# Kernel optimization log

Hardware: AMD Instinct MI355X
Metric: run time of the kernel (lower is better)

The kernel has to match this reference:

```python
import jax, jax.numpy as jnp
import numpy as np

B, N, D, W = 4, 4096, 256, 7
K = 2 * W + 1  # 15 taps: positions [i-2w, ..., i]
H = 4 * D
EPS = 1e-5


def layer_norm(x, g, b):
    mu = jnp.mean(x, axis=-1, keepdims=True)
    var = jnp.mean(jnp.square(x - mu), axis=-1, keepdims=True)
    return (x - mu) * jax.lax.rsqrt(var + EPS) * g + b


def setup_inputs() -> dict:
    key = jax.random.key(0)
    ks = jax.random.split(key, 8)
    s = 0.02
    return {
        "x": jax.random.normal(ks[0], (B, N, D), dtype=jnp.float32),
        # w_mix[k] is the DxD block of the (K*D -> D) Linear acting on offset k-2w
        "w_mix": (jax.random.normal(ks[1], (K, D, D), dtype=jnp.float32) * s),
        "b_mix": jnp.zeros((D,), dtype=jnp.float32),
        "g1": jnp.ones((D,), jnp.float32) + 0.1 * jax.random.normal(ks[2], (D,), jnp.float32),
        "b1": 0.1 * jax.random.normal(ks[3], (D,), jnp.float32),
        "w_ff1": jax.random.normal(ks[4], (D, H), dtype=jnp.float32) * s,
        "b_ff1": jnp.zeros((H,), dtype=jnp.float32),
        "w_ff2": jax.random.normal(ks[5], (H, D), dtype=jnp.float32) * s,
        "b_ff2": jnp.zeros((D,), dtype=jnp.float32),
        "g2": jnp.ones((D,), jnp.float32) + 0.1 * jax.random.normal(ks[6], (D,), jnp.float32),
        "b2": 0.1 * jax.random.normal(ks[7], (D,), jnp.float32),
    }


def reference(x, w_mix, b_mix, g1, b1, w_ff1, b_ff1, w_ff2, b_ff2, g2, b2):
    # Causal windowed concat + Linear == causal 1D conv with kernel K=2w+1.
    # torch feats chunk k holds x[i - 2w + k]; conv tap k with left pad 2w
    # sees exactly x[i - 2w + k], so kernel = mix weight reshaped (K, D, D).
    mix = jax.lax.conv_general_dilated(
        x, w_mix, window_strides=(1,), padding=[(2 * W, 0)],
        dimension_numbers=("NWC", "WIO", "NWC"),
    ) + b_mix  # [B, N, D]
    # Dropout is identity in eval mode (reference baseline).
    h = layer_norm(x + mix, g1, b1)
    ff = jnp.dot(jax.nn.gelu(jnp.dot(h, w_ff1) + b_ff1, approximate=False), w_ff2) + b_ff2
    return layer_norm(h + ff, g2, b2)
```

## Files before the change

kernel.cpp:

```cpp
#include <hip/hip_runtime.h>
#include <cstdint>

#define DD     256
#define HH     1024
#define NNSEQ  4096
#define KDIM   3840
#define NSTEPS 120
#define MT     64
#define XROWS  78
#define XPITCH 264
#define APITCH 136
#define EPSLN  1e-5f

typedef unsigned short u16;
typedef __attribute__((ext_vector_type(8))) short short8;
typedef __attribute__((ext_vector_type(4))) float f32x4;

#define MFMA(a, b, c) __builtin_amdgcn_mfma_f32_16x16x32_bf16(a, b, c, 0, 0, 0)

__device__ __forceinline__ u16 f2bf(float f) {
  unsigned u = __float_as_uint(f);
  u += 0x7FFF + ((u >> 16) & 1);
  return (u16)(u >> 16);
}
__device__ __forceinline__ float bf2f(u16 s) { return __uint_as_float(((unsigned)s) << 16); }

__global__ __launch_bounds__(256) void k_prep(
    const float* __restrict__ wmix, const float* __restrict__ wff1,
    const float* __restrict__ wff2, u16* __restrict__ wpk,
    u16* __restrict__ w1pk, u16* __restrict__ w2pk)
{
  __shared__ float t[32][257];
  const int b = blockIdx.x, tid = threadIdx.x;

  if (b < 120) {
    const int s = b;
    for (int r = 0; r < 32; ++r)
      t[r][tid] = wmix[(size_t)(s * 32 + r) * 256 + tid];
    __syncthreads();
#pragma unroll
    for (int f = 0; f < 4; ++f) {
      const int l = tid & 63, q = l >> 4, cl = l & 15;
      const int nt = (tid >> 6) & 3, ng = f;
      const int n = ng * 64 + nt * 16 + cl;
      uint4 pk;
      unsigned* p = (unsigned*)&pk;
#pragma unroll
      for (int jj = 0; jj < 4; ++jj)
        p[jj] = (unsigned)f2bf(t[q * 8 + jj * 2][n]) | ((unsigned)f2bf(t[q * 8 + jj * 2 + 1][n]) << 16);
      *(uint4*)&wpk[((size_t)s * 1024 + f * 256 + tid) * 8] = pk;
    }
  } else if (b < 184) {
    const int u = b - 120, c = u >> 3, s = u & 7;
    for (int i = 0; i < 16; ++i) {
      const int r = i * 2 + (tid >> 7), col = tid & 127;
      t[r][col] = wff1[(size_t)(s * 32 + r) * 1024 + c * 128 + col];
    }
    __syncthreads();
#pragma unroll
    for (int f = 0; f < 2; ++f) {
      const int l = tid & 63, q = l >> 4, cl = l & 15;
      const int nt = (tid >> 6) & 1, ng = f * 2 + (tid >> 7);
      const int n = ng * 32 + nt * 16 + cl;
      uint4 pk;
      unsigned* p = (unsigned*)&pk;
#pragma unroll
      for (int jj = 0; jj < 4; ++jj)
        p[jj] = (unsigned)f2bf(t[q * 8 + jj * 2][n]) | ((unsigned)f2bf(t[q * 8 + jj * 2 + 1][n]) << 16);
      *(uint4*)&w1pk[((size_t)(c * 8 + s) * 512 + f * 256 + tid) * 8] = pk;
    }
  } else {
    const int u = b - 184, c = u >> 2, s = u & 3;
    for (int r = 0; r < 32; ++r)
      t[r][tid] = wff2[(size_t)(c * 128 + s * 32 + r) * 256 + tid];
    __syncthreads();
#pragma unroll
    for (int f = 0; f < 4; ++f) {
      const int l = tid & 63, q = l >> 4, cl = l & 15;
      const int nt = (tid >> 6) & 3, ng = f;
      const int n = ng * 64 + nt * 16 + cl;
      uint4 pk;
      unsigned* p = (unsigned*)&pk;
#pragma unroll
      for (int jj = 0; jj < 4; ++jj)
        p[jj] = (unsigned)f2bf(t[q * 8 + jj * 2][n]) | ((unsigned)f2bf(t[q * 8 + jj * 2 + 1][n]) << 16);
      *(uint4*)&w2pk[((size_t)(c * 4 + s) * 1024 + f * 256 + tid) * 8] = pk;
    }
  }
}

__global__ __launch_bounds__(512) void k_mix_ln1(
    const float* __restrict__ x, const u16* __restrict__ wpk,
    const float* __restrict__ bmix, const float* __restrict__ g1,
    const float* __restrict__ b1, u16* __restrict__ h)
{
  __shared__ u16 xs[XROWS * XPITCH];
  __shared__ float redS[4][64], redS2[4][64];
  __shared__ float muL[64], invL[64];

  const int tid = threadIdx.x;
  const int wv = tid >> 6, l = tid & 63, q = l >> 4, cl = l & 15;
  const int mg = wv >> 2, ng = wv & 3;
  const long tok0 = (long)blockIdx.x * MT;
  const int n0 = (int)(tok0 & (NNSEQ - 1));

  {
    const int cslot = (tid & 63) * 4;
    for (int r = tid >> 6; r < XROWS; r += 8) {
      const int nloc = n0 - 14 + r;
      float4 v = make_float4(0.f, 0.f, 0.f, 0.f);
      if (nloc >= 0) v = *(const float4*)&x[(tok0 - 14 + r) * DD + cslot];
      uint2 pk;
      pk.x = (unsigned)f2bf(v.x) | ((unsigned)f2bf(v.y) << 16);
      pk.y = (unsigned)f2bf(v.z) | ((unsigned)f2bf(v.w) << 16);
      *(uint2*)&xs[r * XPITCH + cslot] = pk;
    }
  }
  __syncthreads();

  f32x4 acc[2][4];
#pragma unroll
  for (int nt = 0; nt < 4; ++nt) {
    const float bm = bmix[ng * 64 + nt * 16 + cl];
#pragma unroll
    for (int mt = 0; mt < 2; ++mt) acc[mt][nt] = (f32x4){bm, bm, bm, bm};
  }

  const u16* bbase = wpk + (size_t)(ng * 4) * 512 + (size_t)l * 8;

#define LOAD_A(dst, s_)                                                        \
  {                                                                            \
    const int xrow = (s_) >> 3, c0 = ((s_) & 7) * 32;                          \
    _Pragma("unroll")                                                          \
    for (int mt = 0; mt < 2; ++mt)                                             \
      dst[mt] = *(const short8*)&xs[(xrow + mg * 32 + mt * 16 + cl) * XPITCH + c0 + q * 8]; \
  }
#define LOAD_B(dst, s_)                                                        \
  {                                                                            \
    const u16* bp = bbase + (size_t)(s_) * 8192;                               \
    _Pragma("unroll")                                                          \
    for (int nt = 0; nt < 4; ++nt)                                             \
      dst[nt] = *(const short8*)(bp + nt * 512);                               \
  }

  short8 af[3][2], bfr[3][4];
  LOAD_A(af[0], 0) LOAD_B(bfr[0], 0)
  LOAD_A(af[1], 1) LOAD_B(bfr[1], 1)
  LOAD_A(af[2], 2) LOAD_B(bfr[2], 2)

#pragma unroll 3
  for (int s = 0; s < NSTEPS; ++s) {
    const int cur = s % 3;
#pragma unroll
    for (int mt = 0; mt < 2; ++mt)
#pragma unroll
      for (int nt = 0; nt < 4; ++nt)
        acc[mt][nt] = MFMA(af[cur][mt], bfr[cur][nt], acc[mt][nt]);
    if (s + 3 < NSTEPS) {
      LOAD_A(af[cur], s + 3)
      LOAD_B(bfr[cur], s + 3)
    }
  }

#pragma unroll
  for (int mt = 0; mt < 2; ++mt)
#pragma unroll
    for (int nt = 0; nt < 4; ++nt) {
      const int col = ng * 64 + nt * 16 + cl;
#pragma unroll
      for (int reg = 0; reg < 4; ++reg) {
        const int row = mg * 32 + mt * 16 + q * 4 + reg;
        acc[mt][nt][reg] += x[(tok0 + row) * DD + col];
      }
    }

  float ps[2][4], ps2[2][4];
#pragma unroll
  for (int mt = 0; mt < 2; ++mt)
#pragma unroll
    for (int reg = 0; reg < 4; ++reg) {
      float s = 0.f, s2 = 0.f;
#pragma unroll
      for (int nt = 0; nt < 4; ++nt) { const float y = acc[mt][nt][reg]; s += y; s2 += y * y; }
#pragma unroll
      for (int off = 1; off < 16; off <<= 1) { s += __shfl_xor(s, off, 64); s2 += __shfl_xor(s2, off, 64); }
      ps[mt][reg] = s; ps2[mt][reg] = s2;
    }
  if (cl == 0) {
#pragma unroll
    for (int mt = 0; mt < 2; ++mt)
#pragma unroll
      for (int reg = 0; reg < 4; ++reg) {
        const int row = mg * 32 + mt * 16 + q * 4 + reg;
        redS[ng][row] = ps[mt][reg]; redS2[ng][row] = ps2[mt][reg];
      }
  }
  __syncthreads();
  if (tid < 64) {
    const float s  = redS[0][tid] + redS[1][tid] + redS[2][tid] + redS[3][tid];
    const float s2 = redS2[0][tid] + redS2[1][tid] + redS2[2][tid] + redS2[3][tid];
    const float mu = s * (1.f / DD);
    const float var = s2 * (1.f / DD) - mu * mu;
    muL[tid] = mu; invL[tid] = rsqrtf(var + EPSLN);
  }
  __syncthreads();

#pragma unroll
  for (int nt = 0; nt < 4; ++nt) {
    const int col = ng * 64 + nt * 16 + cl;
    const float gv = g1[col], bv = b1[col];
#pragma unroll
    for (int mt = 0; mt < 2; ++mt)
#pragma unroll
      for (int reg = 0; reg < 4; ++reg) {
        const int row = mg * 32 + mt * 16 + q * 4 + reg;
        const float hv = (acc[mt][nt][reg] - muL[row]) * invL[row] * gv + bv;
        h[(tok0 + row) * DD + col] = f2bf(hv);
      }
  }
#undef LOAD_A
#undef LOAD_B
}

__global__ __launch_bounds__(512) void k_ffn_ln2(
    const u16* __restrict__ h, const u16* __restrict__ w1pk,
    const float* __restrict__ bf1, const u16* __restrict__ w2pk,
    const float* __restrict__ bf2, const float* __restrict__ g2,
    const float* __restrict__ b2, float* __restrict__ out)
{
  __shared__ u16 hs[64 * XPITCH];
  __shared__ u16 asb[64 * APITCH];
  __shared__ float redS[4][64], redS2[4][64];
  __shared__ float muL[64], invL[64];

  const int tid = threadIdx.x;
  const int wv = tid >> 6, l = tid & 63, q = l >> 4, cl = l & 15;
  const int mg = wv >> 2, ng = wv & 3;
  const long tok0 = (long)blockIdx.x * MT;

  {
    const int chunk = tid & 31;
#pragma unroll
    for (int i = 0; i < 4; ++i) {
      const int row = (tid >> 5) + i * 16;
      const uint4 v = *(const uint4*)&h[(tok0 + row) * DD + chunk * 8];
      *(uint4*)&hs[row * XPITCH + chunk * 8] = v;
    }
  }
  __syncthreads();

  f32x4 acc2[2][4];
#pragma unroll
  for (int nt = 0; nt < 4; ++nt) {
    const float bv = bf2[ng * 64 + nt * 16 + cl];
#pragma unroll
    for (int mt = 0; mt < 2; ++mt) acc2[mt][nt] = (f32x4){bv, bv, bv, bv};
  }

  for (int c = 0; c < 8; ++c) {
    f32x4 acc1[2][2];
#pragma unroll
    for (int nt = 0; nt < 2; ++nt) {
      const float bv = bf1[c * 128 + ng * 32 + nt * 16 + cl];
#pragma unroll
      for (int mt = 0; mt < 2; ++mt) acc1[mt][nt] = (f32x4){bv, bv, bv, bv};
    }
#pragma unroll
    for (int s = 0; s < 8; ++s) {
      short8 a[2], b[2];
#pragma unroll
      for (int mt = 0; mt < 2; ++mt)
        a[mt] = *(const short8*)&hs[(mg * 32 + mt * 16 + cl) * XPITCH + s * 32 + q * 8];
      const u16* bp = w1pk + ((size_t)((c * 8 + s) * 4 + ng) * 2) * 512 + (size_t)l * 8;
#pragma unroll
      for (int nt = 0; nt < 2; ++nt)
        b[nt] = *(const short8*)(bp + nt * 512);
#pragma unroll
      for (int mt = 0; mt < 2; ++mt)
#pragma unroll
        for (int nt = 0; nt < 2; ++nt)
          acc1[mt][nt] = MFMA(a[mt], b[nt], acc1[mt][nt]);
    }
#pragma unroll
    for (int mt = 0; mt < 2; ++mt)
#pragma unroll
      for (int nt = 0; nt < 2; ++nt)
#pragma unroll
        for (int reg = 0; reg < 4; ++reg) {
          const float v = acc1[mt][nt][reg];
          const float g = 0.5f * v * (1.f + erff(v * 0.70710678118654752f));
          asb[(mg * 32 + mt * 16 + q * 4 + reg) * APITCH + ng * 32 + nt * 16 + cl] = f2bf(g);
        }
    __syncthreads();
#pragma unroll
    for (int s = 0; s < 4; ++s) {
      short8 a[2], b[4];
#pragma unroll
      for (int mt = 0; mt < 2; ++mt)
        a[mt] = *(const short8*)&asb[(mg * 32 + mt * 16 + cl) * APITCH + s * 32 + q * 8];
      const u16* bp = w2pk + ((size_t)((c * 4 + s) * 4 + ng) * 4) * 512 + (size_t)l * 8;
#pragma unroll
      for (int nt = 0; nt < 4; ++nt)
        b[nt] = *(const short8*)(bp + nt * 512);
#pragma unroll
      for (int mt = 0; mt < 2; ++mt)
#pragma unroll
        for (int nt = 0; nt < 4; ++nt)
          acc2[mt][nt] = MFMA(a[mt], b[nt], acc2[mt][nt]);
    }
    __syncthreads();
  }

#pragma unroll
  for (int mt = 0; mt < 2; ++mt)
#pragma unroll
    for (int nt = 0; nt < 4; ++nt) {
      const int col = ng * 64 + nt * 16 + cl;
#pragma unroll
      for (int reg = 0; reg < 4; ++reg) {
        const int row = mg * 32 + mt * 16 + q * 4 + reg;
        acc2[mt][nt][reg] += bf2f(hs[row * XPITCH + col]);
      }
    }

  float ps[2][4], ps2[2][4];
#pragma unroll
  for (int mt = 0; mt < 2; ++mt)
#pragma unroll
    for (int reg = 0; reg < 4; ++reg) {
      float s = 0.f, s2 = 0.f;
#pragma unroll
      for (int nt = 0; nt < 4; ++nt) { const float y = acc2[mt][nt][reg]; s += y; s2 += y * y; }
#pragma unroll
      for (int off = 1; off < 16; off <<= 1) { s += __shfl_xor(s, off, 64); s2 += __shfl_xor(s2, off, 64); }
      ps[mt][reg] = s; ps2[mt][reg] = s2;
    }
  if (cl == 0) {
#pragma unroll
    for (int mt = 0; mt < 2; ++mt)
#pragma unroll
      for (int reg = 0; reg < 4; ++reg) {
        const int row = mg * 32 + mt * 16 + q * 4 + reg;
        redS[ng][row] = ps[mt][reg]; redS2[ng][row] = ps2[mt][reg];
      }
  }
  __syncthreads();
  if (tid < 64) {
    const float s  = redS[0][tid] + redS[1][tid] + redS[2][tid] + redS[3][tid];
    const float s2 = redS2[0][tid] + redS2[1][tid] + redS2[2][tid] + redS2[3][tid];
    const float mu = s * (1.f / DD);
    const float var = s2 * (1.f / DD) - mu * mu;
    muL[tid] = mu; invL[tid] = rsqrtf(var + EPSLN);
  }
  __syncthreads();

#pragma unroll
  for (int nt = 0; nt < 4; ++nt) {
    const int col = ng * 64 + nt * 16 + cl;
    const float gv = g2[col], bv = b2[col];
#pragma unroll
    for (int mt = 0; mt < 2; ++mt)
#pragma unroll
      for (int reg = 0; reg < 4; ++reg) {
        const int row = mg * 32 + mt * 16 + q * 4 + reg;
        out[(tok0 + row) * DD + col] = (acc2[mt][nt][reg] - muL[row]) * invL[row] * gv + bv;
      }
  }
}

extern "C" void kernel_launch(void* const* d_in, const int* in_sizes, int n_in,
                              void* d_out, int out_size, void* d_ws, size_t ws_size,
                              hipStream_t stream) {
  const float* x    = (const float*)d_in[0];
  const float* wmix = (const float*)d_in[1];
  const float* bmix = (const float*)d_in[2];
  const float* g1   = (const float*)d_in[3];
  const float* b1   = (const float*)d_in[4];
  const float* wff1 = (const float*)d_in[5];
  const float* bff1 = (const float*)d_in[6];
  const float* wff2 = (const float*)d_in[7];
  const float* bff2 = (const float*)d_in[8];
  const float* g2   = (const float*)d_in[9];
  const float* b2   = (const float*)d_in[10];
  float* out = (float*)d_out;

  u16* wpk  = (u16*)d_ws;
  u16* w1pk = wpk + 983040;
  u16* w2pk = w1pk + 262144;
  u16* hb   = w2pk + 262144;

  k_prep<<<216, 256, 0, stream>>>(wmix, wff1, wff2, wpk, w1pk, w2pk);

  const int R = 4 * NNSEQ;
  k_mix_ln1 <<<R / MT, 512, 0, stream>>>(x, wpk, bmix, g1, b1, hb);
  k_ffn_ln2 <<<R / MT, 512, 0, stream>>>(hb, w1pk, bff1, w2pk, bff2, g2, b2, out);
}
```

Measured before the change: 174.0 us.

## Use four waves per block, each covering all 64 rows to reuse B fragments

Both fused kernels drop from 512 to 256 threads. Each of the 4 waves now owns a 64-column slice across all 64 rows, instead of 8 waves splitting rows into two groups. This halves the global weight-fragment loads per block, since each B fragment now feeds 4 row tiles instead of 2. The cost is doubled accumulator and A-fragment registers per wave and fewer waves per block to hide latency.

Measured after the change: 186.9 us. 1.07x slower.

```diff
diff --git a/kernel.cpp b/kernel.cpp
--- a/kernel.cpp
+++ b/kernel.cpp
@@ -89,7 +89,7 @@
   }
 }
 
-__global__ __launch_bounds__(512) void k_mix_ln1(
+__global__ __launch_bounds__(256) void k_mix_ln1(
     const float* __restrict__ x, const u16* __restrict__ wpk,
     const float* __restrict__ bmix, const float* __restrict__ g1,
     const float* __restrict__ b1, u16* __restrict__ h)
@@ -99,14 +99,13 @@
   __shared__ float muL[64], invL[64];
 
   const int tid = threadIdx.x;
-  const int wv = tid >> 6, l = tid & 63, q = l >> 4, cl = l & 15;
-  const int mg = wv >> 2, ng = wv & 3;
+  const int ng = tid >> 6, l = tid & 63, q = l >> 4, cl = l & 15;
   const long tok0 = (long)blockIdx.x * MT;
   const int n0 = (int)(tok0 & (NNSEQ - 1));
 
   {
     const int cslot = (tid & 63) * 4;
-    for (int r = tid >> 6; r < XROWS; r += 8) {
+    for (int r = tid >> 6; r < XROWS; r += 4) {
       const int nloc = n0 - 14 + r;
       float4 v = make_float4(0.f, 0.f, 0.f, 0.f);
       if (nloc >= 0) v = *(const float4*)&x[(tok0 - 14 + r) * DD + cslot];
@@ -118,22 +117,22 @@
   }
   __syncthreads();
 
-  f32x4 acc[2][4];
+  f32x4 acc[4][4];
 #pragma unroll
   for (int nt = 0; nt < 4; ++nt) {
     const float bm = bmix[ng * 64 + nt * 16 + cl];
 #pragma unroll
-    for (int mt = 0; mt < 2; ++mt) acc[mt][nt] = (f32x4){bm, bm, bm, bm};
-  }
-
-  const u16* bbase = wpk + (size_t)(ng * 4) * 512 + (size_t)l * 8;
+    for (int mt = 0; mt < 4; ++mt) acc[mt][nt] = (f32x4){bm, bm, bm, bm};
+  }
+
+  const u16* bbase = wpk + (size_t)ng * 2048 + (size_t)l * 8;
 
 #define LOAD_A(dst, s_)                                                        \
   {                                                                            \
     const int xrow = (s_) >> 3, c0 = ((s_) & 7) * 32;                          \
     _Pragma("unroll")                                                          \
-    for (int mt = 0; mt < 2; ++mt)                                             \
-      dst[mt] = *(const short8*)&xs[(xrow + mg * 32 + mt * 16 + cl) * XPITCH + c0 + q * 8]; \
+    for (int mt = 0; mt < 4; ++mt)                                             \
+      dst[mt] = *(const short8*)&xs[(xrow + mt * 16 + cl) * XPITCH + c0 + q * 8]; \
   }
 #define LOAD_B(dst, s_)                                                        \
   {                                                                            \
@@ -143,7 +142,7 @@
       dst[nt] = *(const short8*)(bp + nt * 512);                               \
   }
 
-  short8 af[3][2], bfr[3][4];
+  short8 af[3][4], bfr[3][4];
   LOAD_A(af[0], 0) LOAD_B(bfr[0], 0)
   LOAD_A(af[1], 1) LOAD_B(bfr[1], 1)
   LOAD_A(af[2], 2) LOAD_B(bfr[2], 2)
@@ -152,7 +151,7 @@
   for (int s = 0; s < NSTEPS; ++s) {
     const int cur = s % 3;
 #pragma unroll
-    for (int mt = 0; mt < 2; ++mt)
+    for (int mt = 0; mt < 4; ++mt)
 #pragma unroll
       for (int nt = 0; nt < 4; ++nt)
         acc[mt][nt] = MFMA(af[cur][mt], bfr[cur][nt], acc[mt][nt]);
@@ -161,22 +160,24 @@
       LOAD_B(bfr[cur], s + 3)
     }
   }
-
-#pragma unroll
-  for (int mt = 0; mt < 2; ++mt)
+#undef LOAD_A
+#undef LOAD_B
+
+#pragma unroll
+  for (int mt = 0; mt < 4; ++mt)
 #pragma unroll
     for (int nt = 0; nt < 4; ++nt) {
       const int col = ng * 64 + nt * 16 + cl;
 #pragma unroll
       for (int reg = 0; reg < 4; ++reg) {
-        const int row = mg * 32 + mt * 16 + q * 4 + reg;
+        const int row = mt * 16 + q * 4 + reg;
         acc[mt][nt][reg] += x[(tok0 + row) * DD + col];
       }
     }
 
-  float ps[2][4], ps2[2][4];
-#pragma unroll
-  for (int mt = 0; mt < 2; ++mt)
+  float ps[4][4], ps2[4][4];
+#pragma unroll
+  for (int mt = 0; mt < 4; ++mt)
 #pragma unroll
     for (int reg = 0; reg < 4; ++reg) {
       float s = 0.f, s2 = 0.f;
@@ -188,10 +189,10 @@
     }
   if (cl == 0) {
 #pragma unroll
-    for (int mt = 0; mt < 2; ++mt)
-#pragma unroll
-      for (int reg = 0; reg < 4; ++reg) {
-        const int row = mg * 32 + mt * 16 + q * 4 + reg;
+    for (int mt = 0; mt < 4; ++mt)
+#pragma unroll
+      for (int reg = 0; reg < 4; ++reg) {
+        const int row = mt * 16 + q * 4 + reg;
         redS[ng][row] = ps[mt][reg]; redS2[ng][row] = ps2[mt][reg];
       }
   }
@@ -210,19 +211,17 @@
     const int col = ng * 64 + nt * 16 + cl;
     const float gv = g1[col], bv = b1[col];
 #pragma unroll
-    for (int mt = 0; mt < 2; ++mt)
-#pragma unroll
-      for (int reg = 0; reg < 4; ++reg) {
-        const int row = mg * 32 + mt * 16 + q * 4 + reg;
+    for (int mt = 0; mt < 4; ++mt)
+#pragma unroll
+      for (int reg = 0; reg < 4; ++reg) {
+        const int row = mt * 16 + q * 4 + reg;
         const float hv = (acc[mt][nt][reg] - muL[row]) * invL[row] * gv + bv;
         h[(tok0 + row) * DD + col] = f2bf(hv);
       }
   }
-#undef LOAD_A
-#undef LOAD_B
-}
-
-__global__ __launch_bounds__(512) void k_ffn_ln2(
+}
+
+__global__ __launch_bounds__(256) void k_ffn_ln2(
     const u16* __restrict__ h, const u16* __restrict__ w1pk,
     const float* __restrict__ bf1, const u16* __restrict__ w2pk,
     const float* __restrict__ bf2, const float* __restrict__ g2,
@@ -234,76 +233,75 @@
   __shared__ float muL[64], invL[64];
 
   const int tid = threadIdx.x;
-  const int wv = tid >> 6, l = tid & 63, q = l >> 4, cl = l & 15;
-  const int mg = wv >> 2, ng = wv & 3;
+  const int ng = tid >> 6, l = tid & 63, q = l >> 4, cl = l & 15;
   const long tok0 = (long)blockIdx.x * MT;
 
   {
     const int chunk = tid & 31;
 #pragma unroll
-    for (int i = 0; i < 4; ++i) {
-      const int row = (tid >> 5) + i * 16;
+    for (int i = 0; i < 8; ++i) {
+      const int row = (tid >> 5) + i * 8;
       const uint4 v = *(const uint4*)&h[(tok0 + row) * DD + chunk * 8];
       *(uint4*)&hs[row * XPITCH + chunk * 8] = v;
     }
   }
   __syncthreads();
 
-  f32x4 acc2[2][4];
+  f32x4 acc2[4][4];
 #pragma unroll
   for (int nt = 0; nt < 4; ++nt) {
     const float bv = bf2[ng * 64 + nt * 16 + cl];
 #pragma unroll
-    for (int mt = 0; mt < 2; ++mt) acc2[mt][nt] = (f32x4){bv, bv, bv, bv};
+    for (int mt = 0; mt < 4; ++mt) acc2[mt][nt] = (f32x4){bv, bv, bv, bv};
   }
 
   for (int c = 0; c < 8; ++c) {
-    f32x4 acc1[2][2];
+    f32x4 acc1[4][2];
 #pragma unroll
     for (int nt = 0; nt < 2; ++nt) {
       const float bv = bf1[c * 128 + ng * 32 + nt * 16 + cl];
 #pragma unroll
-      for (int mt = 0; mt < 2; ++mt) acc1[mt][nt] = (f32x4){bv, bv, bv, bv};
+      for (int mt = 0; mt < 4; ++mt) acc1[mt][nt] = (f32x4){bv, bv, bv, bv};
     }
 #pragma unroll
     for (int s = 0; s < 8; ++s) {
-      short8 a[2], b[2];
-#pragma unroll
-      for (int mt = 0; mt < 2; ++mt)
-        a[mt] = *(const short8*)&hs[(mg * 32 + mt * 16 + cl) * XPITCH + s * 32 + q * 8];
-      const u16* bp = w1pk + ((size_t)((c * 8 + s) * 4 + ng) * 2) * 512 + (size_t)l * 8;
+      short8 a[4], b[2];
+#pragma unroll
+      for (int mt = 0; mt < 4; ++mt)
+        a[mt] = *(const short8*)&hs[(mt * 16 + cl) * XPITCH + s * 32 + q * 8];
+      const u16* bp = w1pk + (size_t)(c * 8 + s) * 4096 + ng * 1024 + (size_t)l * 8;
 #pragma unroll
       for (int nt = 0; nt < 2; ++nt)
         b[nt] = *(const short8*)(bp + nt * 512);
 #pragma unroll
-      for (int mt = 0; mt < 2; ++mt)
+      for (int mt = 0; mt < 4; ++mt)
 #pragma unroll
         for (int nt = 0; nt < 2; ++nt)
           acc1[mt][nt] = MFMA(a[mt], b[nt], acc1[mt][nt]);
     }
 #pragma unroll
-    for (int mt = 0; mt < 2; ++mt)
+    for (int mt = 0; mt < 4; ++mt)
 #pragma unroll
       for (int nt = 0; nt < 2; ++nt)
 #pragma unroll
         for (int reg = 0; reg < 4; ++reg) {
           const float v = acc1[mt][nt][reg];
           const float g = 0.5f * v * (1.f + erff(v * 0.70710678118654752f));
-          asb[(mg * 32 + mt * 16 + q * 4 + reg) * APITCH + ng * 32 + nt * 16 + cl] = f2bf(g);
+          asb[(mt * 16 + q * 4 + reg) * APITCH + ng * 32 + nt * 16 + cl] = f2bf(g);
         }
     __syncthreads();
 #pragma unroll
     for (int s = 0; s < 4; ++s) {
-      short8 a[2], b[4];
-#pragma unroll
-      for (int mt = 0; mt < 2; ++mt)
-        a[mt] = *(const short8*)&asb[(mg * 32 + mt * 16 + cl) * APITCH + s * 32 + q * 8];
-      const u16* bp = w2pk + ((size_t)((c * 4 + s) * 4 + ng) * 4) * 512 + (size_t)l * 8;
+      short8 a[4], b[4];
+#pragma unroll
+      for (int mt = 0; mt < 4; ++mt)
+        a[mt] = *(const short8*)&asb[(mt * 16 + cl) * APITCH + s * 32 + q * 8];
+      const u16* bp = w2pk + (size_t)(c * 4 + s) * 8192 + ng * 2048 + (size_t)l * 8;
 #pragma unroll
       for (int nt = 0; nt < 4; ++nt)
         b[nt] = *(const short8*)(bp + nt * 512);
 #pragma unroll
-      for (int mt = 0; mt < 2; ++mt)
+      for (int mt = 0; mt < 4; ++mt)
 #pragma unroll
         for (int nt = 0; nt < 4; ++nt)
           acc2[mt][nt] = MFMA(a[mt], b[nt], acc2[mt][nt]);
@@ -312,20 +310,20 @@
   }
 
 #pragma unroll
-  for (int mt = 0; mt < 2; ++mt)
+  for (int mt = 0; mt < 4; ++mt)
 #pragma unroll
     for (int nt = 0; nt < 4; ++nt) {
       const int col = ng * 64 + nt * 16 + cl;
 #pragma unroll
       for (int reg = 0; reg < 4; ++reg) {
-        const int row = mg * 32 + mt * 16 + q * 4 + reg;
+        const int row = mt * 16 + q * 4 + reg;
         acc2[mt][nt][reg] += bf2f(hs[row * XPITCH + col]);
       }
     }
 
-  float ps[2][4], ps2[2][4];
-#pragma unroll
-  for (int mt = 0; mt < 2; ++mt)
+  float ps[4][4], ps2[4][4];
+#pragma unroll
+  for (int mt = 0; mt < 4; ++mt)
 #pragma unroll
     for (int reg = 0; reg < 4; ++reg) {
       float s = 0.f, s2 = 0.f;
@@ -337,10 +335,10 @@
     }
   if (cl == 0) {
 #pragma unroll
-    for (int mt = 0; mt < 2; ++mt)
-#pragma unroll
-      for (int reg = 0; reg < 4; ++reg) {
-        const int row = mg * 32 + mt * 16 + q * 4 + reg;
+    for (int mt = 0; mt < 4; ++mt)
+#pragma unroll
+      for (int reg = 0; reg < 4; ++reg) {
+        const int row = mt * 16 + q * 4 + reg;
         redS[ng][row] = ps[mt][reg]; redS2[ng][row] = ps2[mt][reg];
       }
   }
@@ -359,10 +357,10 @@
     const int col = ng * 64 + nt * 16 + cl;
     const float gv = g2[col], bv = b2[col];
 #pragma unroll
-    for (int mt = 0; mt < 2; ++mt)
-#pragma unroll
-      for (int reg = 0; reg < 4; ++reg) {
-        const int row = mg * 32 + mt * 16 + q * 4 + reg;
+    for (int mt = 0; mt < 4; ++mt)
+#pragma unroll
+      for (int reg = 0; reg < 4; ++reg) {
+        const int row = mt * 16 + q * 4 + reg;
         out[(tok0 + row) * DD + col] = (acc2[mt][nt][reg] - muL[row]) * invL[row] * gv + bv;
       }
   }
@@ -392,6 +390,6 @@
   k_prep<<<216, 256, 0, stream>>>(wmix, wff1, wff2, wpk, w1pk, w2pk);
 
   const int R = 4 * NNSEQ;
-  k_mix_ln1 <<<R / MT, 512, 0, stream>>>(x, wpk, bmix, g1, b1, hb);
-  k_ffn_ln2 <<<R / MT, 512, 0, stream>>>(hb, w1pk, bff1, w2pk, bff2, g2, b2, out);
-}
+  k_mix_ln1 <<<R / MT, 256, 0, stream>>>(x, wpk, bmix, g1, b1, hb);
+  k_ffn_ln2 <<<R / MT, 256, 0, stream>>>(hb, w1pk, bff1, w2pk, bff2, g2, b2, out);
+}
```

## Fuse mix+LN1 and FFN+LN2 into one kernel with unified weight packing

Applied to the files above, without the earlier changes.

Merges the two main kernels so the LN1 output h stays in shared memory as bf16 and feeds the FFN directly. This removes the global write and read of h and one kernel launch. The FFN hidden dimension is now processed in chunks of 256 instead of 128, and all three weight packings share one 256-column layout and one code path in the prep kernel. Launch bounds now request 2 blocks per CU, which caps register use. Shared memory per block grows, which may limit occupancy and cause spills.

After: 168.1 us. 1.03x faster.

```diff
diff --git a/kernel.cpp b/kernel.cpp
--- a/kernel.cpp
+++ b/kernel.cpp
@@ -9,7 +9,6 @@
 #define MT     64
 #define XROWS  78
 #define XPITCH 264
-#define APITCH 136
 #define EPSLN  1e-5f
 
 typedef unsigned short u16;
@@ -33,68 +32,48 @@
   __shared__ float t[32][257];
   const int b = blockIdx.x, tid = threadIdx.x;
 
+  u16* dst;
   if (b < 120) {
-    const int s = b;
+    dst = wpk + (size_t)b * 8192;
     for (int r = 0; r < 32; ++r)
-      t[r][tid] = wmix[(size_t)(s * 32 + r) * 256 + tid];
-    __syncthreads();
-#pragma unroll
-    for (int f = 0; f < 4; ++f) {
-      const int l = tid & 63, q = l >> 4, cl = l & 15;
-      const int nt = (tid >> 6) & 3, ng = f;
-      const int n = ng * 64 + nt * 16 + cl;
-      uint4 pk;
-      unsigned* p = (unsigned*)&pk;
-#pragma unroll
-      for (int jj = 0; jj < 4; ++jj)
-        p[jj] = (unsigned)f2bf(t[q * 8 + jj * 2][n]) | ((unsigned)f2bf(t[q * 8 + jj * 2 + 1][n]) << 16);
-      *(uint4*)&wpk[((size_t)s * 1024 + f * 256 + tid) * 8] = pk;
-    }
-  } else if (b < 184) {
+      t[r][tid] = wmix[(size_t)(b * 32 + r) * 256 + tid];
+  } else if (b < 152) {
     const int u = b - 120, c = u >> 3, s = u & 7;
-    for (int i = 0; i < 16; ++i) {
-      const int r = i * 2 + (tid >> 7), col = tid & 127;
-      t[r][col] = wff1[(size_t)(s * 32 + r) * 1024 + c * 128 + col];
-    }
-    __syncthreads();
-#pragma unroll
-    for (int f = 0; f < 2; ++f) {
-      const int l = tid & 63, q = l >> 4, cl = l & 15;
-      const int nt = (tid >> 6) & 1, ng = f * 2 + (tid >> 7);
-      const int n = ng * 32 + nt * 16 + cl;
-      uint4 pk;
-      unsigned* p = (unsigned*)&pk;
-#pragma unroll
-      for (int jj = 0; jj < 4; ++jj)
-        p[jj] = (unsigned)f2bf(t[q * 8 + jj * 2][n]) | ((unsigned)f2bf(t[q * 8 + jj * 2 + 1][n]) << 16);
-      *(uint4*)&w1pk[((size_t)(c * 8 + s) * 512 + f * 256 + tid) * 8] = pk;
-    }
+    dst = w1pk + (size_t)u * 8192;
+    for (int r = 0; r < 32; ++r)
+      t[r][tid] = wff1[(size_t)(s * 32 + r) * 1024 + c * 256 + tid];
   } else {
-    const int u = b - 184, c = u >> 2, s = u & 3;
+    const int u = b - 152, c = u >> 3, s = u & 7;
+    dst = w2pk + (size_t)u * 8192;
     for (int r = 0; r < 32; ++r)
-      t[r][tid] = wff2[(size_t)(c * 128 + s * 32 + r) * 256 + tid];
-    __syncthreads();
-#pragma unroll
-    for (int f = 0; f < 4; ++f) {
-      const int l = tid & 63, q = l >> 4, cl = l & 15;
-      const int nt = (tid >> 6) & 3, ng = f;
-      const int n = ng * 64 + nt * 16 + cl;
-      uint4 pk;
-      unsigned* p = (unsigned*)&pk;
-#pragma unroll
-      for (int jj = 0; jj < 4; ++jj)
-        p[jj] = (unsigned)f2bf(t[q * 8 + jj * 2][n]) | ((unsigned)f2bf(t[q * 8 + jj * 2 + 1][n]) << 16);
-      *(uint4*)&w2pk[((size_t)(c * 4 + s) * 1024 + f * 256 + tid) * 8] = pk;
-    }
+      t[r][tid] = wff2[(size_t)(c * 256 + s * 32 + r) * 256 + tid];
+  }
+  __syncthreads();
+
+  const int l = tid & 63, q = l >> 4, cl = l & 15;
+#pragma unroll
+  for (int f = 0; f < 4; ++f) {
+    const int fi = f * 4 + (tid >> 6);
+    const int n = fi * 16 + cl;
+    uint4 pk;
+    unsigned* p = (unsigned*)&pk;
+#pragma unroll
+    for (int jj = 0; jj < 4; ++jj)
+      p[jj] = (unsigned)f2bf(t[q * 8 + jj * 2][n]) | ((unsigned)f2bf(t[q * 8 + jj * 2 + 1][n]) << 16);
+    *(uint4*)&dst[(size_t)fi * 512 + l * 8] = pk;
   }
 }
 
-__global__ __launch_bounds__(512) void k_mix_ln1(
+__global__ __launch_bounds__(512, 2) void k_fused(
     const float* __restrict__ x, const u16* __restrict__ wpk,
     const float* __restrict__ bmix, const float* __restrict__ g1,
-    const float* __restrict__ b1, u16* __restrict__ h)
+    const float* __restrict__ b1, const u16* __restrict__ w1pk,
+    const float* __restrict__ bf1, const u16* __restrict__ w2pk,
+    const float* __restrict__ bf2, const float* __restrict__ g2,
+    const float* __restrict__ b2, float* __restrict__ out)
 {
-  __shared__ u16 xs[XROWS * XPITCH];
+  __shared__ u16 smA[XROWS * XPITCH];
+  __shared__ u16 asb[64 * XPITCH];
   __shared__ float redS[4][64], redS2[4][64];
   __shared__ float muL[64], invL[64];
 
@@ -113,7 +92,7 @@
       uint2 pk;
       pk.x = (unsigned)f2bf(v.x) | ((unsigned)f2bf(v.y) << 16);
       pk.y = (unsigned)f2bf(v.z) | ((unsigned)f2bf(v.w) << 16);
-      *(uint2*)&xs[r * XPITCH + cslot] = pk;
+      *(uint2*)&smA[r * XPITCH + cslot] = pk;
     }
   }
   __syncthreads();
@@ -126,14 +105,14 @@
     for (int mt = 0; mt < 2; ++mt) acc[mt][nt] = (f32x4){bm, bm, bm, bm};
   }
 
-  const u16* bbase = wpk + (size_t)(ng * 4) * 512 + (size_t)l * 8;
+  const u16* bbase = wpk + (size_t)ng * 2048 + (size_t)l * 8;
 
 #define LOAD_A(dst, s_)                                                        \
   {                                                                            \
     const int xrow = (s_) >> 3, c0 = ((s_) & 7) * 32;                          \
     _Pragma("unroll")                                                          \
     for (int mt = 0; mt < 2; ++mt)                                             \
-      dst[mt] = *(const short8*)&xs[(xrow + mg * 32 + mt * 16 + cl) * XPITCH + c0 + q * 8]; \
+      dst[mt] = *(const short8*)&smA[(xrow + mg * 32 + mt * 16 + cl) * XPITCH + c0 + q * 8]; \
   }
 #define LOAD_B(dst, s_)                                                        \
   {                                                                            \
@@ -143,24 +122,28 @@
       dst[nt] = *(const short8*)(bp + nt * 512);                               \
   }
 
-  short8 af[3][2], bfr[3][4];
-  LOAD_A(af[0], 0) LOAD_B(bfr[0], 0)
-  LOAD_A(af[1], 1) LOAD_B(bfr[1], 1)
-  LOAD_A(af[2], 2) LOAD_B(bfr[2], 2)
+  {
+    short8 af[3][2], bfr[3][4];
+    LOAD_A(af[0], 0) LOAD_B(bfr[0], 0)
+    LOAD_A(af[1], 1) LOAD_B(bfr[1], 1)
+    LOAD_A(af[2], 2) LOAD_B(bfr[2], 2)
 
 #pragma unroll 3
-  for (int s = 0; s < NSTEPS; ++s) {
-    const int cur = s % 3;
-#pragma unroll
-    for (int mt = 0; mt < 2; ++mt)
-#pragma unroll
-      for (int nt = 0; nt < 4; ++nt)
-        acc[mt][nt] = MFMA(af[cur][mt], bfr[cur][nt], acc[mt][nt]);
-    if (s + 3 < NSTEPS) {
-      LOAD_A(af[cur], s + 3)
-      LOAD_B(bfr[cur], s + 3)
-    }
-  }
+    for (int s = 0; s < NSTEPS; ++s) {
+      const int cur = s % 3;
+#pragma unroll
+      for (int mt = 0; mt < 2; ++mt)
+#pragma unroll
+        for (int nt = 0; nt < 4; ++nt)
+          acc[mt][nt] = MFMA(af[cur][mt], bfr[cur][nt], acc[mt][nt]);
+      if (s + 3 < NSTEPS) {
+        LOAD_A(af[cur], s + 3)
+        LOAD_B(bfr[cur], s + 3)
+      }
+    }
+  }
+#undef LOAD_A
+#undef LOAD_B
 
 #pragma unroll
   for (int mt = 0; mt < 2; ++mt)
@@ -174,26 +157,28 @@
       }
     }
 
-  float ps[2][4], ps2[2][4];
-#pragma unroll
-  for (int mt = 0; mt < 2; ++mt)
-#pragma unroll
-    for (int reg = 0; reg < 4; ++reg) {
-      float s = 0.f, s2 = 0.f;
-#pragma unroll
-      for (int nt = 0; nt < 4; ++nt) { const float y = acc[mt][nt][reg]; s += y; s2 += y * y; }
-#pragma unroll
-      for (int off = 1; off < 16; off <<= 1) { s += __shfl_xor(s, off, 64); s2 += __shfl_xor(s2, off, 64); }
-      ps[mt][reg] = s; ps2[mt][reg] = s2;
-    }
-  if (cl == 0) {
-#pragma unroll
-    for (int mt = 0; mt < 2; ++mt)
-#pragma unroll
-      for (int reg = 0; reg < 4; ++reg) {
-        const int row = mg * 32 + mt * 16 + q * 4 + reg;
-        redS[ng][row] = ps[mt][reg]; redS2[ng][row] = ps2[mt][reg];
-      }
+  {
+    float ps[2][4], ps2[2][4];
+#pragma unroll
+    for (int mt = 0; mt < 2; ++mt)
+#pragma unroll
+      for (int reg = 0; reg < 4; ++reg) {
+        float s = 0.f, s2 = 0.f;
+#pragma unroll
+        for (int nt = 0; nt < 4; ++nt) { const float y = acc[mt][nt][reg]; s += y; s2 += y * y; }
+#pragma unroll
+        for (int off = 1; off < 16; off <<= 1) { s += __shfl_xor(s, off, 64); s2 += __shfl_xor(s2, off, 64); }
+        ps[mt][reg] = s; ps2[mt][reg] = s2;
+      }
+    if (cl == 0) {
+#pragma unroll
+      for (int mt = 0; mt < 2; ++mt)
+#pragma unroll
+        for (int reg = 0; reg < 4; ++reg) {
+          const int row = mg * 32 + mt * 16 + q * 4 + reg;
+          redS[ng][row] = ps[mt][reg]; redS2[ng][row] = ps2[mt][reg];
+        }
+    }
   }
   __syncthreads();
   if (tid < 64) {
@@ -215,37 +200,8 @@
       for (int reg = 0; reg < 4; ++reg) {
         const int row = mg * 32 + mt * 16 + q * 4 + reg;
         const float hv = (acc[mt][nt][reg] - muL[row]) * invL[row] * gv + bv;
-        h[(tok0 + row) * DD + col] = f2bf(hv);
-      }
-  }
-#undef LOAD_A
-#undef LOAD_B
-}
-
-__global__ __launch_bounds__(512) void k_ffn_ln2(
-    const u16* __restrict__ h, const u16* __restrict__ w1pk,
-    const float* __restrict__ bf1, const u16* __restrict__ w2pk,
-    const float* __restrict__ bf2, const float* __restrict__ g2,
-    const float* __restrict__ b2, float* __restrict__ out)
-{
-  __shared__ u16 hs[64 * XPITCH];
-  __shared__ u16 asb[64 * APITCH];
-  __shared__ float redS[4][64], redS2[4][64];
-  __shared__ float muL[64], invL[64];
-
-  const int tid = threadIdx.x;
-  const int wv = tid >> 6, l = tid & 63, q = l >> 4, cl = l & 15;
-  const int mg = wv >> 2, ng = wv & 3;
-  const long tok0 = (long)blockIdx.x * MT;
-
-  {
-    const int chunk = tid & 31;
-#pragma unroll
-    for (int i = 0; i < 4; ++i) {
-      const int row = (tid >> 5) + i * 16;
-      const uint4 v = *(const uint4*)&h[(tok0 + row) * DD + chunk * 8];
-      *(uint4*)&hs[row * XPITCH + chunk * 8] = v;
-    }
+        smA[row * XPITCH + col] = f2bf(hv);
+      }
   }
   __syncthreads();
 
@@ -257,48 +213,48 @@
     for (int mt = 0; mt < 2; ++mt) acc2[mt][nt] = (f32x4){bv, bv, bv, bv};
   }
 
-  for (int c = 0; c < 8; ++c) {
-    f32x4 acc1[2][2];
-#pragma unroll
-    for (int nt = 0; nt < 2; ++nt) {
-      const float bv = bf1[c * 128 + ng * 32 + nt * 16 + cl];
+  for (int c = 0; c < 4; ++c) {
+    f32x4 acc1[2][4];
+#pragma unroll
+    for (int nt = 0; nt < 4; ++nt) {
+      const float bv = bf1[c * 256 + ng * 64 + nt * 16 + cl];
 #pragma unroll
       for (int mt = 0; mt < 2; ++mt) acc1[mt][nt] = (f32x4){bv, bv, bv, bv};
     }
 #pragma unroll
     for (int s = 0; s < 8; ++s) {
-      short8 a[2], b[2];
-#pragma unroll
-      for (int mt = 0; mt < 2; ++mt)
-        a[mt] = *(const short8*)&hs[(mg * 32 + mt * 16 + cl) * XPITCH + s * 32 + q * 8];
-      const u16* bp = w1pk + ((size_t)((c * 8 + s) * 4 + ng) * 2) * 512 + (size_t)l * 8;
-#pragma unroll
-      for (int nt = 0; nt < 2; ++nt)
+      short8 a[2], b[4];
+#pragma unroll
+      for (int mt = 0; mt < 2; ++mt)
+        a[mt] = *(const short8*)&smA[(mg * 32 + mt * 16 + cl) * XPITCH + s * 32 + q * 8];
+      const u16* bp = w1pk + (size_t)(c * 8 + s) * 8192 + ng * 2048 + (size_t)l * 8;
+#pragma unroll
+      for (int nt = 0; nt < 4; ++nt)
         b[nt] = *(const short8*)(bp + nt * 512);
 #pragma unroll
       for (int mt = 0; mt < 2; ++mt)
 #pragma unroll
-        for (int nt = 0; nt < 2; ++nt)
+        for (int nt = 0; nt < 4; ++nt)
           acc1[mt][nt] = MFMA(a[mt], b[nt], acc1[mt][nt]);
     }
 #pragma unroll
     for (int mt = 0; mt < 2; ++mt)
 #pragma unroll
-      for (int nt = 0; nt < 2; ++nt)
+      for (int nt = 0; nt < 4; ++nt)
 #pragma unroll
         for (int reg = 0; reg < 4; ++reg) {
           const float v = acc1[mt][nt][reg];
           const float g = 0.5f * v * (1.f + erff(v * 0.70710678118654752f));
-          asb[(mg * 32 + mt * 16 + q * 4 + reg) * APITCH + ng * 32 + nt * 16 + cl] = f2bf(g);
+          asb[(mg * 32 + mt * 16 + q * 4 + reg) * XPITCH + ng * 64 + nt * 16 + cl] = f2bf(g);
         }
     __syncthreads();
 #pragma unroll
-    for (int s = 0; s < 4; ++s) {
+    for (int s = 0; s < 8; ++s) {
       short8 a[2], b[4];
 #pragma unroll
       for (int mt = 0; mt < 2; ++mt)
-        a[mt] = *(const short8*)&asb[(mg * 32 + mt * 16 + cl) * APITCH + s * 32 + q * 8];
-      const u16* bp = w2pk + ((size_t)((c * 4 + s) * 4 + ng) * 4) * 512 + (size_t)l * 8;
+        a[mt] = *(const short8*)&asb[(mg * 32 + mt * 16 + cl) * XPITCH + s * 32 + q * 8];
+      const u16* bp = w2pk + (size_t)(c * 8 + s) * 8192 + ng * 2048 + (size_t)l * 8;
 #pragma unroll
       for (int nt = 0; nt < 4; ++nt)
         b[nt] = *(const short8*)(bp + nt * 512);
@@ -319,30 +275,32 @@
 #pragma unroll
       for (int reg = 0; reg < 4; ++reg) {
         const int row = mg * 32 + mt * 16 + q * 4 + reg;
-        acc2[mt][nt][reg] += bf2f(hs[row * XPITCH + col]);
-      }
-    }
-
-  float ps[2][4], ps2[2][4];
-#pragma unroll
-  for (int mt = 0; mt < 2; ++mt)
-#pragma unroll
-    for (int reg = 0; reg < 4; ++reg) {
-      float s = 0.f, s2 = 0.f;
-#pragma unroll
-      for (int nt = 0; nt < 4; ++nt) { const float y = acc2[mt][nt][reg]; s += y; s2 += y * y; }
-#pragma unroll
-      for (int off = 1; off < 16; off <<= 1) { s += __shfl_xor(s, off, 64); s2 += __shfl_xor(s2, off, 64); }
-      ps[mt][reg] = s; ps2[mt][reg] = s2;
-    }
-  if (cl == 0) {
-#pragma unroll
-    for (int mt = 0; mt < 2; ++mt)
-#pragma unroll
-      for (int reg = 0; reg < 4; ++reg) {
-        const int row = mg * 32 + mt * 16 + q * 4 + reg;
-        redS[ng][row] = ps[mt][reg]; redS2[ng][row] = ps2[mt][reg];
-      }
+        acc2[mt][nt][reg] += bf2f(smA[row * XPITCH + col]);
+      }
+    }
+
+  {
+    float ps[2][4], ps2[2][4];
+#pragma unroll
+    for (int mt = 0; mt < 2; ++mt)
+#pragma unroll
+      for (int reg = 0; reg < 4; ++reg) {
+        float s = 0.f, s2 = 0.f;
+#pragma unroll
+        for (int nt = 0; nt < 4; ++nt) { const float y = acc2[mt][nt][reg]; s += y; s2 += y * y; }
+#pragma unroll
+        for (int off = 1; off < 16; off <<= 1) { s += __shfl_xor(s, off, 64); s2 += __shfl_xor(s2, off, 64); }
+        ps[mt][reg] = s; ps2[mt][reg] = s2;
+      }
+    if (cl == 0) {
+#pragma unroll
+      for (int mt = 0; mt < 2; ++mt)
+#pragma unroll
+        for (int reg = 0; reg < 4; ++reg) {
+          const int row = mg * 32 + mt * 16 + q * 4 + reg;
+          redS[ng][row] = ps[mt][reg]; redS2[ng][row] = ps2[mt][reg];
+        }
+    }
   }
   __syncthreads();
   if (tid < 64) {
@@ -387,11 +345,10 @@
   u16* wpk  = (u16*)d_ws;
   u16* w1pk = wpk + 983040;
   u16* w2pk = w1pk + 262144;
-  u16* hb   = w2pk + 262144;
-
-  k_prep<<<216, 256, 0, stream>>>(wmix, wff1, wff2, wpk, w1pk, w2pk);
+
+  k_prep<<<184, 256, 0, stream>>>(wmix, wff1, wff2, wpk, w1pk, w2pk);
 
   const int R = 4 * NNSEQ;
-  k_mix_ln1 <<<R / MT, 512, 0, stream>>>(x, wpk, bmix, g1, b1, hb);
-  k_ffn_ln2 <<<R / MT, 512, 0, stream>>>(hb, w1pk, bff1, w2pk, bff2, g2, b2, out);
+  k_fused<<<R / MT, 512, 0, stream>>>(x, wpk, bmix, g1, b1,
+                                      w1pk, bff1, w2pk, bff2, g2, b2, out);
 }
```
